# Kernel tuning notes

Measured on AMD Instinct MI355X. Metric: run time of the kernel, lower is better.

The kernel has to match this reference:

```python
import jax, jax.numpy as jnp
import numpy as np

DIM = 256


def _layernorm(x, g, b, eps=1e-5):
    mu = x.mean(-1, keepdims=True)
    var = x.var(-1, keepdims=True)  # biased, matches torch LayerNorm
    return (x - mu) / jnp.sqrt(var + eps) * g + b


def _softmax_kernel(d, proj, ratio, eps=1e-4):
    # FAVOR+ softmax kernel feature map: ratio*(exp(d@proj^T - |d|^2/2) + eps)
    dd = jnp.einsum('bnc,fc->bnf', d, proj)
    diag = 0.5 * jnp.sum(d * d, axis=-1, keepdims=True)
    return ratio * (jnp.exp(dd - diag) + eps)


def setup_inputs() -> dict:
    d = DIM
    rng = np.random.default_rng(0)
    # gaussian orthogonal random matrix (nb_features == dim -> single QR block)
    qmat, _ = np.linalg.qr(rng.standard_normal((d, d)))
    mult = np.linalg.norm(rng.standard_normal((d, d)), axis=1)
    proj = (np.diag(mult) @ qmat.T).astype(np.float32)

    key = jax.random.key(0)
    ks = jax.random.split(key, 8)

    def lin(k, o, i):
        s = 1.0 / np.sqrt(i)
        return jax.random.uniform(k, (o, i), jnp.float32, -s, s)

    return {
        'x': jax.random.normal(ks[0], (8, d, 64, 64), jnp.float32),
        'proj': jnp.asarray(proj),
        'wq': lin(ks[1], d, d), 'bq': jnp.zeros((d,), jnp.float32),
        'wk': lin(ks[2], d, d), 'bk': jnp.zeros((d,), jnp.float32),
        'wa': lin(ks[3], d, d), 'ba': jnp.zeros((d,), jnp.float32),
        'g1': jnp.ones((d,), jnp.float32), 'b1': jnp.zeros((d,), jnp.float32),
        'g2': jnp.ones((d,), jnp.float32), 'b2': jnp.zeros((d,), jnp.float32),
        'w1': lin(ks[4], 4 * d, d), 'fb1': jnp.zeros((4 * d,), jnp.float32),
        'w2': lin(ks[5], d, 4 * d), 'fb2': jnp.zeros((d,), jnp.float32),
    }


def reference(x, proj, wq, bq, wk, bk, wa, ba, g1, b1, g2, b2, w1, fb1, w2, fb2):
    B, C, H, W = x.shape
    N = H * W
    t = x.reshape(B, C, N).transpose(0, 2, 1)  # [B, N, C] tokens
    shortcut = t
    h = _layernorm(t, g1, b1)
    # 1x1 convs == per-token linears (conv weight [out,in,1,1] -> [out,in])
    q = h @ wq.T + bq
    k = h @ wk.T + bk
    v = h @ wa.T + ba
    # F.normalize(p=2, dim=channel, eps=5e-5): x / max(||x||, eps)
    qn = q / jnp.maximum(jnp.linalg.norm(q, axis=-1, keepdims=True), 5e-5)
    kn = k / jnp.maximum(jnp.linalg.norm(k, axis=-1, keepdims=True), 5e-5)
    ratio = proj.shape[0] ** -0.5
    qp = _softmax_kernel(qn, proj, ratio)  # [B, N, F]
    kp = _softmax_kernel(kn, proj, ratio)  # [B, N, F]
    # linear attention (single head, squeezed)
    k_sum = kp.sum(axis=1)                                    # [B, F]
    D_inv = 1.0 / jnp.einsum('bnf,bf->bn', qp, k_sum)         # [B, N]
    ctx = jnp.einsum('bnf,bnc->bfc', kp, v)                   # [B, F, C]
    out = jnp.einsum('bfc,bnf,bn->bnc', ctx, qp, D_inv)       # [B, N, C]
    t = shortcut + out
    h2 = _layernorm(t, g2, b2)
    m = jax.nn.gelu(h2 @ w1.T + fb1, approximate=False) @ w2.T + fb2
    t = t + m
    return t.transpose(0, 2, 1).reshape(B, C, H, W)
```

## Files before the change

### kernel.cpp

```cpp
#include <hip/hip_runtime.h>
#include <hip/hip_bf16.h>
#include <math.h>

typedef __hip_bfloat16 bf16;
typedef __attribute__((ext_vector_type(8))) short short8;
typedef __attribute__((ext_vector_type(4))) short short4v;
typedef __attribute__((ext_vector_type(4))) unsigned short ushort4v;
typedef __attribute__((ext_vector_type(4))) float f32x4;
typedef unsigned int u32;

#define BB 8
#define CC 256
#define NTOKB 4096
#define FF 256
#define HIDDEN 1024
#define NTOK (BB*NTOKB)

#if defined(__has_builtin)
#if __has_builtin(__builtin_amdgcn_global_load_lds)
#define HAS_GLL 1
#endif
#endif
#ifndef HAS_GLL
#define HAS_GLL 0
#endif

__device__ __forceinline__ float bf2f(bf16 x) { return __bfloat162float(x); }
__device__ __forceinline__ bf16 f2bf(float x) { return __float2bfloat16(x); }
__device__ __forceinline__ float clampf(float v, float lo, float hi) {
    return fminf(fmaxf(v, lo), hi);
}
__device__ __forceinline__ float s2f(short s) {
    unsigned int u = ((unsigned int)(unsigned short)s) << 16;
    float f; __builtin_memcpy(&f, &u, 4); return f;
}
__device__ __forceinline__ unsigned short f2bits(float v) {
    bf16 h = f2bf(v);
    unsigned short b; __builtin_memcpy(&b, &h, 2); return b;
}

__device__ __forceinline__ float fast_erf(float x) {
    float ax = fabsf(x);
    float t = __builtin_amdgcn_rcpf(fmaf(0.3275911f, ax, 1.f));
    float p = fmaf(t, 1.061405429f, -1.453152027f);
    p = fmaf(t, p, 1.421413741f);
    p = fmaf(t, p, -0.284496736f);
    p = fmaf(t, p, 0.254829592f);
    p = p * t;
    float e = __expf(-ax * ax);
    float r = fmaf(-p, e, 1.f);
    return x < 0.f ? -r : r;
}

#if HAS_GLL
__device__ __forceinline__ void gll16(const void* g, void* l) {
    __builtin_amdgcn_global_load_lds(
        (const __attribute__((address_space(1))) u32*)g,
        (__attribute__((address_space(3))) u32*)l, 16, 0, 0);
}
#endif

__device__ __forceinline__ float ldin(const void* p, size_t i, int fp32mode) {
    float v = fp32mode ? ((const float*)p)[i] : __bfloat162float(((const bf16*)p)[i]);
    if (!(v == v)) v = 0.f;
    return clampf(v, -1e4f, 1e4f);
}

__device__ __forceinline__ float wave_sum(float v) {
#pragma unroll
    for (int off = 32; off > 0; off >>= 1) v += __shfl_xor(v, off, 64);
    return v;
}

__global__ void detect_mode(const void* __restrict__ x, int* __restrict__ flag) {
    int i = threadIdx.x;
    float vb = __bfloat162float(((const bf16*)x)[(size_t)i * 37 + 1]);
    int bad = (!(vb == vb)) || (fabsf(vb) > 1e4f);
    unsigned long long m = __ballot(bad);
    if (i == 0) *flag = (m != 0ull) ? 1 : 0;
}

__global__ void convw_all(const void* __restrict__ wq, const void* __restrict__ wk,
                          const void* __restrict__ wa, const void* __restrict__ proj,
                          const void* __restrict__ w1, const void* __restrict__ w2,
                          const void* __restrict__ bq, const void* __restrict__ bk,
                          const void* __restrict__ ba,
                          bf16* __restrict__ dst, float* __restrict__ bqkv,
                          const int* __restrict__ mode) {
    int fp32 = *mode;
    int i = blockIdx.x * 256 + threadIdx.x;
    if (i < 786432) {
        const void* src; size_t off;
        if (i < 262144) {
            int seg = i >> 16; off = (size_t)(i & 65535);
            src = seg == 0 ? wq : seg == 1 ? wk : seg == 2 ? wa : proj;
        } else if (i < 524288) { src = w1; off = (size_t)(i - 262144); }
        else { src = w2; off = (size_t)(i - 524288); }
        dst[i] = f2bf(ldin(src, off, fp32));
    } else if (i < 787200) {
        int j = i - 786432;
        const void* s = j < 256 ? bq : j < 512 ? bk : ba;
        bqkv[j] = ldin(s, (size_t)(j & 255), fp32);
    }
}


__global__ void transpose_in_off(const void* __restrict__ X, bf16* __restrict__ T,
                                 const int* __restrict__ mode, size_t eoff) {
    __shared__ float tile[32][33];
    int fp32 = *mode;
    int n0 = blockIdx.x * 32, c0 = blockIdx.y * 32;
    int tx = threadIdx.x, ty = threadIdx.y;
    for (int i = ty; i < 32; i += 8)
        tile[i][tx] = ldin(X, eoff + (size_t)(c0 + i) * NTOKB + n0 + tx, fp32);
    __syncthreads();
    for (int i = ty; i < 32; i += 8)
        T[(size_t)(n0 + i) * CC + c0 + tx] = f2bf(tile[tx][i]);
}

__global__ void transpose_out_off(const bf16* __restrict__ T, void* __restrict__ O,
                                  const int* __restrict__ mode, size_t eoff) {
    __shared__ float tile[32][33];
    int fp32 = *mode;
    int c0 = blockIdx.x * 32, n0 = blockIdx.y * 32;
    int tx = threadIdx.x, ty = threadIdx.y;
    for (int i = ty; i < 32; i += 8)
        tile[i][tx] = bf2f(T[(size_t)(n0 + i) * CC + c0 + tx]);
    __syncthreads();
    for (int i = ty; i < 32; i += 8) {
        size_t idx = eoff + (size_t)(c0 + i) * NTOKB + n0 + tx;
        float v = tile[tx][i];
        if (fp32) ((float*)O)[idx] = v; else ((bf16*)O)[idx] = f2bf(v);
    }
}

__global__ void transpose_in_z(const void* __restrict__ X, bf16* __restrict__ T,
                               const int* __restrict__ mode) {
    __shared__ float tile[32][33];
    int fp32 = *mode;
    int b = blockIdx.z;
    int n0 = blockIdx.x * 32, c0 = blockIdx.y * 32;
    int tx = threadIdx.x, ty = threadIdx.y;
    size_t eoff = (size_t)b * CC * NTOKB;
    for (int i = ty; i < 32; i += 8)
        tile[i][tx] = ldin(X, eoff + (size_t)(c0 + i) * NTOKB + n0 + tx, fp32);
    __syncthreads();
    for (int i = ty; i < 32; i += 8)
        T[((size_t)b * NTOKB + n0 + i) * CC + c0 + tx] = f2bf(tile[tx][i]);
}

__global__ void layernorm_k(const bf16* __restrict__ X, const void* __restrict__ g,
                            const void* __restrict__ bta, bf16* __restrict__ Y,
                            const int* __restrict__ mode) {
    int fp32 = *mode;
    int t = blockIdx.x * 4 + (threadIdx.x >> 6);
    int lane = threadIdx.x & 63;
    const bf16* row = X + (size_t)t * CC;
    float v[4], s = 0.f, s2 = 0.f;
#pragma unroll
    for (int j = 0; j < 4; j++) {
        v[j] = bf2f(row[lane + 64 * j]);
        s += v[j]; s2 += v[j] * v[j];
    }
    s = wave_sum(s); s2 = wave_sum(s2);
    float mu = s * (1.f / CC);
    float var = s2 * (1.f / CC) - mu * mu;
    float rstd = rsqrtf(fmaxf(var, 0.f) + 1e-5f);
    bf16* yrow = Y + (size_t)t * CC;
#pragma unroll
    for (int j = 0; j < 4; j++) {
        int c = lane + 64 * j;
        yrow[c] = f2bf((v[j] - mu) * rstd * ldin(g, c, fp32) + ldin(bta, c, fp32));
    }
}

__global__ void layernorm_v(const bf16* __restrict__ X, const void* __restrict__ g,
                            const void* __restrict__ bta, bf16* __restrict__ Y,
                            const int* __restrict__ mode) {
    int fp32 = *mode;
    int t = blockIdx.x * 4 + (threadIdx.x >> 6);
    int lane = threadIdx.x & 63;
    const short* row = (const short*)X + (size_t)t * CC;
    short4v u = *(const short4v*)&row[lane * 4];
    float v[4], s = 0.f, s2 = 0.f;
#pragma unroll
    for (int j = 0; j < 4; j++) { v[j] = s2f(u[j]); s += v[j]; s2 += v[j] * v[j]; }
    s = wave_sum(s); s2 = wave_sum(s2);
    float mu = s * (1.f / CC);
    float var = s2 * (1.f / CC) - mu * mu;
    float rstd = rsqrtf(fmaxf(var, 0.f) + 1e-5f);
    ushort4v o;
#pragma unroll
    for (int j = 0; j < 4; j++) {
        int c = lane * 4 + j;
        o[j] = f2bits((v[j] - mu) * rstd * ldin(g, c, fp32) + ldin(bta, c, fp32));
    }
    *(ushort4v*)((unsigned short*)Y + (size_t)t * CC + lane * 4) = o;
}

__global__ void rownorm_k(bf16* __restrict__ Q, float* __restrict__ DIAG) {
    int t = blockIdx.x * 4 + (threadIdx.x >> 6);
    int lane = threadIdx.x & 63;
    bf16* row = Q + (size_t)t * CC;
    float v[4], s2 = 0.f;
#pragma unroll
    for (int j = 0; j < 4; j++) { v[j] = bf2f(row[lane + 64 * j]); s2 += v[j] * v[j]; }
    s2 = wave_sum(s2);
    float nrm = sqrtf(fmaxf(s2, 0.f));
    float scale = 1.f / fmaxf(nrm, 5e-5f);
#pragma unroll
    for (int j = 0; j < 4; j++) row[lane + 64 * j] = f2bf(v[j] * scale);
    if (lane == 0) DIAG[t] = 0.5f * s2 * scale * scale;
}

__global__ void rownorm_v(bf16* __restrict__ Q, float* __restrict__ DIAG) {
    int t = blockIdx.x * 4 + (threadIdx.x >> 6);
    int lane = threadIdx.x & 63;
    short* row = (short*)Q + (size_t)t * CC;
    short4v u = *(const short4v*)&row[lane * 4];
    float v[4], s2 = 0.f;
#pragma unroll
    for (int j = 0; j < 4; j++) { v[j] = s2f(u[j]); s2 += v[j] * v[j]; }
    s2 = wave_sum(s2);
    float nrm = sqrtf(fmaxf(s2, 0.f));
    float scale = 1.f / fmaxf(nrm, 5e-5f);
    ushort4v o;
#pragma unroll
    for (int j = 0; j < 4; j++) o[j] = f2bits(v[j] * scale);
    *(ushort4v*)&row[lane * 4] = o;
    if (lane == 0) DIAG[t] = 0.5f * s2 * scale * scale;
}


template <int EPI>
__global__ void gemm_nt(const bf16* __restrict__ A, const void* __restrict__ Bw,
                        const void* __restrict__ bias, const float* __restrict__ diag,
                        const bf16* __restrict__ resid, bf16* __restrict__ Cm,
                        int M, int Nn, int Kk, const int* __restrict__ mode) {
    __shared__ float As[32][33];
    __shared__ float Bs[32][33];
    int fp32 = *mode;
    int tx = threadIdx.x, ty = threadIdx.y;
    int n0 = blockIdx.x * 32, m0 = blockIdx.y * 32;
    int tid = ty * 16 + tx;
    int lr = tid >> 5, lc = tid & 31;
    float acc[2][2] = {{0.f, 0.f}, {0.f, 0.f}};
    for (int k0 = 0; k0 < Kk; k0 += 32) {
#pragma unroll
        for (int i = 0; i < 4; i++) {
            int r = lr + 8 * i;
            As[r][lc] = bf2f(A[(size_t)(m0 + r) * Kk + k0 + lc]);
            Bs[r][lc] = ldin(Bw, (size_t)(n0 + r) * Kk + k0 + lc, fp32);
        }
        __syncthreads();
#pragma unroll
        for (int kk = 0; kk < 32; kk++) {
            float a0 = As[ty][kk], a1 = As[ty + 16][kk];
            float b0 = Bs[tx][kk], b1 = Bs[tx + 16][kk];
            acc[0][0] += a0 * b0; acc[0][1] += a0 * b1;
            acc[1][0] += a1 * b0; acc[1][1] += a1 * b1;
        }
        __syncthreads();
    }
#pragma unroll
    for (int i = 0; i < 2; i++)
#pragma unroll
        for (int j = 0; j < 2; j++) {
            int m = m0 + ty + 16 * i, n = n0 + tx + 16 * j;
            float v = acc[i][j];
            if (EPI == 0) {
                v = clampf(v + ldin(bias, n, fp32), -1e6f, 1e6f);
            } else if (EPI == 1) {
                v = fminf(0.0625f * (expf(fminf(v - diag[m], 60.f)) + 1e-4f), 1e8f);
            } else if (EPI == 2) {
                v += ldin(bias, n, fp32);
                v = 0.5f * v * (1.f + erff(v * 0.70710678118654752f));
            } else if (EPI == 3) {
                v += ldin(bias, n, fp32);
                v = clampf(v + bf2f(resid[(size_t)m * Nn + n]), -1e6f, 1e6f);
            }
            Cm[(size_t)m * Nn + n] = f2bf(v);
        }
}

__global__ void gemm_ctx_fb(const bf16* __restrict__ KP, const bf16* __restrict__ V,
                            float* __restrict__ CTX) {
    __shared__ float Ks[32][33];
    __shared__ float Vs[32][33];
    int c0 = blockIdx.x * 32, f0 = blockIdx.y * 32;
    int tx = threadIdx.x, ty = threadIdx.y;
    int tid = ty * 16 + tx, lr = tid >> 5, lc = tid & 31;
    float acc[2][2] = {{0.f, 0.f}, {0.f, 0.f}};
    for (int n0 = 0; n0 < NTOKB; n0 += 32) {
#pragma unroll
        for (int i = 0; i < 4; i++) {
            int r = lr + 8 * i;
            Ks[r][lc] = bf2f(KP[(size_t)(n0 + r) * FF + f0 + lc]);
            Vs[r][lc] = bf2f(V[(size_t)(n0 + r) * CC + c0 + lc]);
        }
        __syncthreads();
#pragma unroll
        for (int kk = 0; kk < 32; kk++) {
            float a0 = Ks[kk][ty], a1 = Ks[kk][ty + 16];
            float b0 = Vs[kk][tx], b1 = Vs[kk][tx + 16];
            acc[0][0] += a0 * b0; acc[0][1] += a0 * b1;
            acc[1][0] += a1 * b0; acc[1][1] += a1 * b1;
        }
        __syncthreads();
    }
#pragma unroll
    for (int i = 0; i < 2; i++)
#pragma unroll
        for (int j = 0; j < 2; j++)
            CTX[(size_t)(f0 + ty + 16 * i) * CC + c0 + tx + 16 * j] =
                clampf(acc[i][j], -1e18f, 1e18f);
}

__global__ void gemm_attnout_fb(const bf16* __restrict__ QP, const float* __restrict__ CTX,
                                const float* __restrict__ DINV, bf16* __restrict__ T) {
    __shared__ float As[32][33];
    __shared__ float Bs[32][33];
    int c0 = blockIdx.x * 32, m0 = blockIdx.y * 32;
    int tx = threadIdx.x, ty = threadIdx.y;
    int tid = ty * 16 + tx, lr = tid >> 5, lc = tid & 31;
    float acc[2][2] = {{0.f, 0.f}, {0.f, 0.f}};
    for (int k0 = 0; k0 < FF; k0 += 32) {
#pragma unroll
        for (int i = 0; i < 4; i++) {
            int r = lr + 8 * i;
            As[r][lc] = bf2f(QP[(size_t)(m0 + r) * FF + k0 + lc]);
            Bs[r][lc] = CTX[(size_t)(k0 + r) * CC + c0 + lc];
        }
        __syncthreads();
#pragma unroll
        for (int kk = 0; kk < 32; kk++) {
            float a0 = As[ty][kk], a1 = As[ty + 16][kk];
            float b0 = Bs[kk][tx], b1 = Bs[kk][tx + 16];
            acc[0][0] += a0 * b0; acc[0][1] += a0 * b1;
            acc[1][0] += a1 * b0; acc[1][1] += a1 * b1;
        }
        __syncthreads();
    }
#pragma unroll
    for (int i = 0; i < 2; i++)
#pragma unroll
        for (int j = 0; j < 2; j++) {
            int t = m0 + ty + 16 * i;
            size_t idx = (size_t)t * CC + c0 + tx + 16 * j;
            float addv = clampf(acc[i][j] * DINV[t], -1e6f, 1e6f);
            T[idx] = f2bf(bf2f(T[idx]) + addv);
        }
}

__global__ void colsum_k(const bf16* __restrict__ KP, float* __restrict__ KPART) {
    int chunk = blockIdx.x;
    int f = threadIdx.x;
    const bf16* base = KP + (size_t)chunk * 128 * FF + f;
    float acc = 0.f;
    for (int i = 0; i < 128; i++) acc += bf2f(base[(size_t)i * FF]);
    KPART[(size_t)chunk * FF + f] = acc;
}

__global__ void ksum_reduce(const float* __restrict__ KPART, float* __restrict__ KSUM) {
    int f = threadIdx.x;
    float acc = 0.f;
#pragma unroll
    for (int c = 0; c < 32; c++) acc += KPART[(size_t)c * FF + f];
    KSUM[f] = acc;
}

__global__ void dinv_k(const bf16* __restrict__ QP, const float* __restrict__ KSUM,
                       float* __restrict__ DINV) {
    int t = blockIdx.x * 4 + (threadIdx.x >> 6);
    int lane = threadIdx.x & 63;
    const bf16* row = QP + (size_t)t * FF;
    float s = 0.f;
#pragma unroll
    for (int j = 0; j < 4; j++) { int c = lane + 64 * j; s += bf2f(row[c]) * KSUM[c]; }
    s = wave_sum(s);
    if (lane == 0) DINV[t] = fminf(1.f / fmaxf(s, 1e-30f), 1e6f);
}

template <int BM, int BN, int EPI, bool TRANSC>
__global__ __launch_bounds__(256) void mgemm(
    const bf16* __restrict__ A, int lda, long long aZ,
    const void* __restrict__ Bv, int ldb, long long bZ,
    const void* __restrict__ bias, const float* __restrict__ diag,
    const float* __restrict__ dinv,
    bf16* __restrict__ Cb, int ldc,
    bf16* __restrict__ Cb2, bf16* __restrict__ Cb3, float* __restrict__ Cf,
    int MperZ, int Kc, int nchunk, const int* __restrict__ mode)
{
    constexpr int MI = BM / 32;
    constexpr int NI = BN / 32;
    __shared__ short As[2][BM][32];
    __shared__ short Bs[2][BN][32];
    int fp32 = *mode;
    int z = blockIdx.z;
    int bl = z / nchunk;
    int chunk = z - bl * nchunk;
    const short* Ag = (const short*)A + (size_t)bl * aZ;
    const short* Bg = (const short*)Bv + (size_t)bl * bZ;

    int bx = blockIdx.x, by = blockIdx.y;
    if ((gridDim.y & 7) == 0) {
        int NB = gridDim.x;
        int flat = by * NB + bx;
        int grp = flat / (8 * NB);
        int rem = flat - grp * 8 * NB;
        by = grp * 8 + (rem & 7);
        bx = rem >> 3;
    }
    int n0 = bx * BN, m0 = by * BM;

    int tid = threadIdx.x;
    int lane = tid & 63, wave = tid >> 6;
    int wm = wave >> 1, wn = wave & 1;
    int row16 = lane & 15, quad = lane >> 4;
    int lrow = lane >> 2, lcol = (lane & 3) * 8;

    f32x4 acc[MI][NI];
#pragma unroll
    for (int i = 0; i < MI; i++)
#pragma unroll
        for (int j = 0; j < NI; j++) acc[i][j] = {0.f, 0.f, 0.f, 0.f};

    const int arb = wave * (BM / 4);
    const int brb = wave * (BN / 4);

    int kBase = chunk * Kc;
    int nt = Kc >> 5;

    auto stage = [&](int b, int kb) {
#pragma unroll
        for (int t = 0; t < BM / 64; t++) {
            int rbase = arb + t * 16;
            const short* gsrc = &Ag[(size_t)(m0 + rbase + lrow) * lda + kb + lcol];
#if HAS_GLL
            gll16(gsrc, &As[b][rbase][0]);
#else
            *(short8*)&As[b][rbase + lrow][lcol] = *(const short8*)gsrc;
#endif
        }
#pragma unroll
        for (int t = 0; t < BN / 64; t++) {
            int rbase = brb + t * 16;
            const short* gsrc = &Bg[(size_t)(n0 + rbase + lrow) * ldb + kb + lcol];
#if HAS_GLL
            gll16(gsrc, &Bs[b][rbase][0]);
#else
            *(short8*)&Bs[b][rbase + lrow][lcol] = *(const short8*)gsrc;
#endif
        }
    };

    auto compute = [&](int b) {
        short8 af[MI], bfr[NI];
#pragma unroll
        for (int i = 0; i < MI; i++)
            af[i] = *(const short8*)&As[b][wm * (BM / 2) + i * 16 + row16][quad * 8];
#pragma unroll
        for (int j = 0; j < NI; j++)
            bfr[j] = *(const short8*)&Bs[b][wn * (BN / 2) + j * 16 + row16][quad * 8];
#pragma unroll
        for (int i = 0; i < MI; i++)
#pragma unroll
            for (int j = 0; j < NI; j++)
                acc[i][j] = __builtin_amdgcn_mfma_f32_16x16x32_bf16(af[i], bfr[j], acc[i][j], 0, 0, 0);
    };

    stage(0, kBase);
    __syncthreads();

    int cur = 0;
    for (int t = 0; t + 1 < nt; ++t) {
        stage(cur ^ 1, kBase + (t + 1) * 32);
        compute(cur);
        __syncthreads();
        cur ^= 1;
    }
    compute(cur);

    float bv[NI];
    if (EPI == 0 || EPI == 2 || EPI == 3 || EPI == 8) {
#pragma unroll
        for (int j = 0; j < NI; j++)
            bv[j] = ldin(bias, n0 + wn * (BN / 2) + j * 16 + row16, fp32);
    } else if (EPI == 6) {
#pragma unroll
        for (int j = 0; j < NI; j++)
            bv[j] = diag[n0 + wn * (BN / 2) + j * 16 + row16];
    } else {
#pragma unroll
        for (int j = 0; j < NI; j++) bv[j] = 0.f;
    }

#pragma unroll
    for (int i = 0; i < MI; i++) {
        int mb = m0 + wm * (BM / 2) + i * 16 + quad * 4;
        float dg[4] = {0.f, 0.f, 0.f, 0.f};
        if (EPI == 1) {
#pragma unroll
            for (int r = 0; r < 4; r++) dg[r] = diag[mb + r];
        }
        if (EPI == 7) {
#pragma unroll
            for (int r = 0; r < 4; r++) dg[r] = diag[(size_t)bl * MperZ + mb + r];
        }
        float dvv[4] = {0.f, 0.f, 0.f, 0.f};
        if (EPI == 5) {
#pragma unroll
            for (int r = 0; r < 4; r++) dvv[r] = dinv[(size_t)bl * MperZ + mb + r];
        }
#pragma unroll
        for (int j = 0; j < NI; j++) {
            int n = n0 + wn * (BN / 2) + j * 16 + row16;
            if (EPI == 6) {
                int seg = n0 >> 8;
                int c = n & 255;
                if (seg == 2) {
                    ushort4v pack;
#pragma unroll
                    for (int r = 0; r < 4; r++)
                        pack[r] = f2bits(clampf(acc[i][j][r] + bv[j], -1e6f, 1e6f));
                    int blq = mb >> 12, tb = mb & 4095;
                    *(ushort4v*)((unsigned short*)Cb3 +
                        (size_t)blq * CC * NTOKB + (size_t)c * NTOKB + tb) = pack;
                } else {
                    bf16* dst = seg ? Cb2 : Cb;
#pragma unroll
                    for (int r = 0; r < 4; r++) {
                        float v = clampf(acc[i][j][r] + bv[j], -1e6f, 1e6f);
                        dst[(size_t)(mb + r) * CC + c] = f2bf(v);
                    }
                }
            } else if (EPI == 7) {
                if (bl == 1) {
                    ushort4v pack;
#pragma unroll
                    for (int r = 0; r < 4; r++) {
                        float v = fminf(0.0625f * (__expf(fminf(acc[i][j][r] - dg[r], 60.f)) + 1e-4f), 1e8f);
                        pack[r] = f2bits(v);
                    }
                    int blq = mb >> 12, tb = mb & 4095;
                    *(ushort4v*)((unsigned short*)Cb2 +
                        (size_t)blq * CC * NTOKB + (size_t)n * NTOKB + tb) = pack;
                } else {
#pragma unroll
                    for (int r = 0; r < 4; r++) {
                        float v = fminf(0.0625f * (__expf(fminf(acc[i][j][r] - dg[r], 60.f)) + 1e-4f), 1e8f);
                        Cb[(size_t)(mb + r) * ldc + n] = f2bf(v);
                    }
                }
            } else if (EPI == 8) {
                int blq = mb >> 12, tb = mb & 4095;
                if (fp32) {
                    f32x4 o;
#pragma unroll
                    for (int r = 0; r < 4; r++) {
                        float v = acc[i][j][r] + bv[j];
                        v = clampf(v + bf2f(Cb[(size_t)(mb + r) * ldc + n]), -1e6f, 1e6f);
                        o[r] = bf2f(f2bf(v));
                    }
                    *(f32x4*)((float*)Cb3 + ((size_t)blq * CC + n) * NTOKB + tb) = o;
                } else {
                    ushort4v pack;
#pragma unroll
                    for (int r = 0; r < 4; r++) {
                        float v = acc[i][j][r] + bv[j];
                        v = clampf(v + bf2f(Cb[(size_t)(mb + r) * ldc + n]), -1e6f, 1e6f);
                        pack[r] = f2bits(v);
                    }
                    *(ushort4v*)((unsigned short*)Cb3 + ((size_t)blq * CC + n) * NTOKB + tb) = pack;
                }
            } else if (TRANSC) {
                ushort4v pack;
#pragma unroll
                for (int r = 0; r < 4; r++) {
                    float v = acc[i][j][r];
                    if (EPI == 0) {
                        v = clampf(v + bv[j], -1e6f, 1e6f);
                    } else {
                        v = fminf(0.0625f * (__expf(fminf(v - dg[r], 60.f)) + 1e-4f), 1e8f);
                    }
                    pack[r] = f2bits(v);
                }
                int blq = mb >> 12, tb = mb & 4095;
                *(ushort4v*)((unsigned short*)Cb +
                    (size_t)blq * CC * NTOKB + (size_t)n * NTOKB + tb) = pack;
            } else {
#pragma unroll
                for (int r = 0; r < 4; r++) {
                    int m = mb + r;
                    float v = acc[i][j][r];
                    if (EPI == 0) {
                        v = clampf(v + bv[j], -1e6f, 1e6f);
                        Cb[(size_t)m * ldc + n] = f2bf(v);
                    } else if (EPI == 1) {
                        v = fminf(0.0625f * (__expf(fminf(v - dg[r], 60.f)) + 1e-4f), 1e8f);
                        Cb[(size_t)m * ldc + n] = f2bf(v);
                    } else if (EPI == 2) {
                        v += bv[j];
                        v = 0.5f * v * (1.f + fast_erf(v * 0.70710678118654752f));
                        Cb[(size_t)m * ldc + n] = f2bf(v);
                    } else if (EPI == 3) {
                        v += bv[j];
                        size_t idx = (size_t)m * ldc + n;
                        v = clampf(v + bf2f(Cb[idx]), -1e6f, 1e6f);
                        Cb[idx] = f2bf(v);
                    } else if (EPI == 4) {
                        Cf[(size_t)z * MperZ + (size_t)m * ldc + n] = v;
                    } else if (EPI == 5) {
                        size_t mg = (size_t)bl * MperZ + m;
                        float addv = clampf(v * dvv[r], -1e6f, 1e6f);
                        size_t idx = mg * ldc + n;
                        Cb[idx] = f2bf(bf2f(Cb[idx]) + addv);
                    }
                }
            }
        }
    }
}

__global__ void reduce_ctx(const float* __restrict__ PART, bf16* __restrict__ CTXT) {
    int f = blockIdx.x;
    int bl = blockIdx.y;
    int c = threadIdx.x;
    float s = 0.f;
#pragma unroll
    for (int ch = 0; ch < 16; ch++)
        s += PART[(((size_t)bl * 16 + ch) * FF + f) * CC + c];
    s = clampf(s, -1e18f, 1e18f);
    CTXT[((size_t)bl * CC + c) * FF + f] = f2bf(s);
}

__global__ void colsum_t(const bf16* __restrict__ KPT, float* __restrict__ KSUM) {
    int bl = blockIdx.y;
    int f = blockIdx.x * 4 + (threadIdx.x >> 6);
    int lane = threadIdx.x & 63;
    const short* row = (const short*)KPT + ((size_t)bl * FF + f) * NTOKB;
    float s = 0.f;
    for (int i = lane * 8; i < NTOKB; i += 512) {
        short8 v = *(const short8*)&row[i];
#pragma unroll
        for (int j = 0; j < 8; j++) s += s2f(v[j]);
    }
    s = wave_sum(s);
    if (lane == 0) KSUM[(size_t)bl * FF + f] = s;
}

__global__ void dinv_v(const bf16* __restrict__ QP, const float* __restrict__ KSUM,
                       float* __restrict__ DINV) {
    int bl = blockIdx.y;
    int t = blockIdx.x * 4 + (threadIdx.x >> 6);
    int lane = threadIdx.x & 63;
    const short* row = (const short*)QP + ((size_t)bl * NTOKB + t) * FF;
    const float* ks = KSUM + (size_t)bl * FF;
    short4v u = *(const short4v*)&row[lane * 4];
    float s = 0.f;
#pragma unroll
    for (int j = 0; j < 4; j++) s += s2f(u[j]) * ks[lane * 4 + j];
    s = wave_sum(s);
    if (lane == 0) DINV[(size_t)bl * NTOKB + t] = fminf(1.f / fmaxf(s, 1e-30f), 1e6f);
}

extern "C" void kernel_launch(void* const* d_in, const int* in_sizes, int n_in,
                              void* d_out, int out_size, void* d_ws, size_t ws_size,
                              hipStream_t stream) {
    const void* x    = d_in[0];
    const void* proj = d_in[1];
    const void* wq   = d_in[2];
    const void* bq   = d_in[3];
    const void* wk   = d_in[4];
    const void* bk   = d_in[5];
    const void* wa   = d_in[6];
    const void* ba   = d_in[7];
    const void* g1   = d_in[8];
    const void* b1   = d_in[9];
    const void* g2   = d_in[10];
    const void* b2   = d_in[11];
    const void* w1   = d_in[12];
    const void* fb1  = d_in[13];
    const void* w2   = d_in[14];
    const void* fb2  = d_in[15];

    char* base = (char*)d_ws;
    const size_t MB = 1048576ull;
    const bool fast = ws_size >= 168 * MB;

    if (fast) {
        bf16* T    = (bf16*)base;
        bf16* Hs   = (bf16*)(base + 16 * MB);
        bf16* Qs   = (bf16*)(base + 32 * MB);
        bf16* Ks   = (bf16*)(base + 48 * MB);
        bf16* VT   = (bf16*)(base + 64 * MB);
        bf16* KPT  = (bf16*)(base + 80 * MB);
        bf16* MID  = (bf16*)(base + 96 * MB);
        float* PART = (float*)(base + 96 * MB);
        char* sm = base + 160 * MB;
        int* MODE = (int*)sm;
        float* DIAGQ = (float*)(sm + 1024);
        float* DIAGK = DIAGQ + NTOK;
        float* DINV  = DIAGK + NTOK;
        float* KSUM  = DINV + NTOK;
        bf16* CTXT   = (bf16*)(sm + 2 * MB);
        bf16* WB     = (bf16*)(sm + 4 * MB);
        float* BQKV  = (float*)(sm + 6 * MB);

        dim3 tb32(32, 8);
        detect_mode<<<1, 64, 0, stream>>>(x, MODE);
        convw_all<<<3075, 256, 0, stream>>>(wq, wk, wa, proj, w1, w2,
                                            bq, bk, ba, WB, BQKV, MODE);
        transpose_in_z<<<dim3(NTOKB / 32, CC / 32, BB), tb32, 0, stream>>>(x, T, MODE);

        layernorm_v<<<NTOK / 4, 256, 0, stream>>>(T, g1, b1, Hs, MODE);
        mgemm<128, 128, 6, false><<<dim3(6, 256, 1), 256, 0, stream>>>(
            Hs, 256, 0, WB, 256, 0, nullptr, BQKV, nullptr,
            Qs, 256, Ks, VT, nullptr, 0, 256, 1, MODE);
        rownorm_v<<<NTOK / 4, 256, 0, stream>>>(Qs, DIAGQ);
        rownorm_v<<<NTOK / 4, 256, 0, stream>>>(Ks, DIAGK);
        mgemm<128, 128, 7, false><<<dim3(2, 256, 2), 256, 0, stream>>>(
            Qs, 256, 8388608LL , WB + 196608, 256, 0,
            nullptr, DIAGQ, nullptr,
            Hs, 256, KPT, nullptr, nullptr, NTOK, 256, 1, MODE);
        bf16* QP = Hs;
        colsum_t<<<dim3(FF / 4, BB), 256, 0, stream>>>(KPT, KSUM);
        dinv_v<<<dim3(NTOKB / 4, BB), 256, 0, stream>>>(QP, KSUM, DINV);
        mgemm<64, 128, 4, false><<<dim3(2, 4, BB * 16), 256, 0, stream>>>(
            KPT, NTOKB, (long long)FF * NTOKB, VT, NTOKB, (long long)CC * NTOKB,
            nullptr, nullptr, nullptr,
            nullptr, CC, nullptr, nullptr, PART, FF * CC, 256, 16, MODE);
        reduce_ctx<<<dim3(FF, BB), 256, 0, stream>>>(PART, CTXT);
        mgemm<128, 64, 5, false><<<dim3(4, 32, BB), 256, 0, stream>>>(
            QP, 256, (long long)NTOKB * FF, CTXT, FF, (long long)CC * FF,
            nullptr, nullptr, DINV,
            T, 256, nullptr, nullptr, nullptr, NTOKB, 256, 1, MODE);
        layernorm_v<<<NTOK / 4, 256, 0, stream>>>(T, g2, b2, Hs, MODE);
        mgemm<128, 128, 2, false><<<dim3(8, 256, 1), 256, 0, stream>>>(
            Hs, 256, 0, WB + 262144, 256, 0, fb1, nullptr, nullptr,
            MID, 1024, nullptr, nullptr, nullptr, 0, 256, 1, MODE);
        mgemm<128, 128, 8, false><<<dim3(2, 256, 1), 256, 0, stream>>>(
            MID, 1024, 0, WB + 524288, 1024, 0, fb2, nullptr, nullptr,
            T, 256, nullptr, (bf16*)d_out, nullptr, 0, 1024, 1, MODE);
        return;
    }

    bf16* Tb   = (bf16*)(base);
    bf16* Hb   = (bf16*)(base + 2 * MB);
    bf16* Qb   = (bf16*)(base + 4 * MB);
    bf16* Kb   = (bf16*)(base + 6 * MB);
    bf16* Vb   = (bf16*)(base + 8 * MB);
    bf16* QPb  = (bf16*)(base + 2 * MB);
    bf16* KPb  = (bf16*)(base + 4 * MB);
    bf16* MIDb = (bf16*)(base + 2 * MB);
    bf16* H2b  = (bf16*)(base + 10 * MB);
    char* sm   = base + 12 * MB;
    int*   MODE  = (int*)sm;
    float* DIAGQ = (float*)(sm + 256);
    float* DIAGK = DIAGQ + NTOKB;
    float* DINV  = DIAGK + NTOKB;
    float* KSUM  = DINV + NTOKB;
    float* KPART = KSUM + FF;
    float* CTX   = KPART + 32 * FF;

    dim3 tb32(32, 8);
    dim3 tb16(16, 16);
    dim3 gq(CC / 32, NTOKB / 32);

    detect_mode<<<1, 64, 0, stream>>>(x, MODE);

    for (int b = 0; b < BB; b++) {
        size_t eoff = (size_t)b * CC * NTOKB;
        transpose_in_off<<<dim3(NTOKB / 32, CC / 32), tb32, 0, stream>>>(x, Tb, MODE, eoff);
        layernorm_k<<<NTOKB / 4, 256, 0, stream>>>(Tb, g1, b1, Hb, MODE);
        gemm_nt<0><<<gq, tb16, 0, stream>>>(Hb, wq, bq, nullptr, nullptr, Qb, NTOKB, CC, CC, MODE);
        gemm_nt<0><<<gq, tb16, 0, stream>>>(Hb, wk, bk, nullptr, nullptr, Kb, NTOKB, CC, CC, MODE);
        gemm_nt<0><<<gq, tb16, 0, stream>>>(Hb, wa, ba, nullptr, nullptr, Vb, NTOKB, CC, CC, MODE);
        rownorm_k<<<NTOKB / 4, 256, 0, stream>>>(Qb, DIAGQ);
        rownorm_k<<<NTOKB / 4, 256, 0, stream>>>(Kb, DIAGK);
        gemm_nt<1><<<gq, tb16, 0, stream>>>(Qb, proj, nullptr, DIAGQ, nullptr, QPb, NTOKB, FF, CC, MODE);
        gemm_nt<1><<<gq, tb16, 0, stream>>>(Kb, proj, nullptr, DIAGK, nullptr, KPb, NTOKB, FF, CC, MODE);
        colsum_k<<<32, 256, 0, stream>>>(KPb, KPART);
        ksum_reduce<<<1, 256, 0, stream>>>(KPART, KSUM);
        dinv_k<<<NTOKB / 4, 256, 0, stream>>>(QPb, KSUM, DINV);
        gemm_ctx_fb<<<dim3(CC / 32, FF / 32), tb16, 0, stream>>>(KPb, Vb, CTX);
        gemm_attnout_fb<<<gq, tb16, 0, stream>>>(QPb, CTX, DINV, Tb);
        layernorm_k<<<NTOKB / 4, 256, 0, stream>>>(Tb, g2, b2, H2b, MODE);
        gemm_nt<2><<<dim3(HIDDEN / 32, NTOKB / 32), tb16, 0, stream>>>(H2b, w1, fb1, nullptr, nullptr, MIDb, NTOKB, HIDDEN, CC, MODE);
        gemm_nt<3><<<gq, tb16, 0, stream>>>(MIDb, w2, fb2, nullptr, Tb, Tb, NTOKB, CC, HIDDEN, MODE);
        transpose_out_off<<<dim3(CC / 32, NTOKB / 32), tb32, 0, stream>>>(Tb, d_out, MODE, eoff);
    }
}
```

Before: 383.6 us.

## Fuse input transpose with layernorm and fold row normalization into feature GEMM

Replaces the separate input transpose and first layernorm with one kernel that loads a 256x32 tile, computes per-token statistics in shared memory, and writes both the token copy and the normalized activations. The q/k row normalization no longer rewrites Q and K. It stores only a per-row scale, which the projection GEMM epilogue applies before the exponential. GEMM staging also uses precomputed incrementing pointers in place of recomputed addresses. This removes a full pass over the activations and two read-modify-write passes, at the cost of a large shared tile per block (about 34KB) that may limit occupancy, and a rounding difference because normalization now happens after the bf16 matmul.

```diff
diff --git a/kernel.cpp b/kernel.cpp
--- a/kernel.cpp
+++ b/kernel.cpp
@@ -104,6 +104,59 @@
     }
 }
 
+__global__ __launch_bounds__(256) void trans_ln(const void* __restrict__ X,
+        const void* __restrict__ g, const void* __restrict__ bta,
+        bf16* __restrict__ T, bf16* __restrict__ H,
+        const int* __restrict__ mode) {
+    __shared__ float tile[CC][33];
+    __shared__ float ps[8][32], ps2[8][32];
+    __shared__ float mu_s[32], rs_s[32];
+    int fp32 = *mode;
+    int b = blockIdx.y;
+    int n0 = blockIdx.x * 32;
+    int tx = threadIdx.x & 31, ty = threadIdx.x >> 5;
+    size_t eoff = (size_t)b * CC * NTOKB;
+    for (int c0 = 0; c0 < CC; c0 += 32)
+        for (int i = ty; i < 32; i += 8)
+            tile[c0 + i][tx] = ldin(X, eoff + (size_t)(c0 + i) * NTOKB + n0 + tx, fp32);
+    __syncthreads();
+    {
+        float s = 0.f, s2 = 0.f;
+#pragma unroll 8
+        for (int c = ty * 32; c < ty * 32 + 32; c++) {
+            float v = tile[c][tx]; s += v; s2 += v * v;
+        }
+        ps[ty][tx] = s; ps2[ty][tx] = s2;
+    }
+    __syncthreads();
+    if (threadIdx.x < 32) {
+        float s = 0.f, s2 = 0.f;
+#pragma unroll
+        for (int p = 0; p < 8; p++) { s += ps[p][threadIdx.x]; s2 += ps2[p][threadIdx.x]; }
+        float mu = s * (1.f / CC);
+        float var = s2 * (1.f / CC) - mu * mu;
+        mu_s[threadIdx.x] = mu;
+        rs_s[threadIdx.x] = rsqrtf(fmaxf(var, 0.f) + 1e-5f);
+    }
+    __syncthreads();
+    int token = threadIdx.x >> 3;
+    int cbase = (threadIdx.x & 7) * 32;
+    float mu = mu_s[token], rstd = rs_s[token];
+    size_t rowoff = ((size_t)b * NTOKB + n0 + token) * CC + cbase;
+    for (int cc = 0; cc < 32; cc += 4) {
+        ushort4v tpack, hpack;
+#pragma unroll
+        for (int q = 0; q < 4; q++) {
+            int c = cbase + cc + q;
+            float v = tile[c][token];
+            tpack[q] = f2bits(v);
+            hpack[q] = f2bits((v - mu) * rstd * ldin(g, c, fp32) + ldin(bta, c, fp32));
+        }
+        *(ushort4v*)((unsigned short*)T + rowoff + cc) = tpack;
+        *(ushort4v*)((unsigned short*)H + rowoff + cc) = hpack;
+    }
+}
+
 
 __global__ void transpose_in_off(const void* __restrict__ X, bf16* __restrict__ T,
                                  const int* __restrict__ mode, size_t eoff) {
@@ -134,21 +187,6 @@
     }
 }
 
-__global__ void transpose_in_z(const void* __restrict__ X, bf16* __restrict__ T,
-                               const int* __restrict__ mode) {
-    __shared__ float tile[32][33];
-    int fp32 = *mode;
-    int b = blockIdx.z;
-    int n0 = blockIdx.x * 32, c0 = blockIdx.y * 32;
-    int tx = threadIdx.x, ty = threadIdx.y;
-    size_t eoff = (size_t)b * CC * NTOKB;
-    for (int i = ty; i < 32; i += 8)
-        tile[i][tx] = ldin(X, eoff + (size_t)(c0 + i) * NTOKB + n0 + tx, fp32);
-    __syncthreads();
-    for (int i = ty; i < 32; i += 8)
-        T[((size_t)b * NTOKB + n0 + i) * CC + c0 + tx] = f2bf(tile[tx][i]);
-}
-
 __global__ void layernorm_k(const bf16* __restrict__ X, const void* __restrict__ g,
                             const void* __restrict__ bta, bf16* __restrict__ Y,
                             const int* __restrict__ mode) {
@@ -213,22 +251,22 @@
     if (lane == 0) DIAG[t] = 0.5f * s2 * scale * scale;
 }
 
-__global__ void rownorm_v(bf16* __restrict__ Q, float* __restrict__ DIAG) {
+__global__ void rowscale_v(const bf16* __restrict__ Q, float* __restrict__ SCALE,
+                           float* __restrict__ DIAG) {
     int t = blockIdx.x * 4 + (threadIdx.x >> 6);
     int lane = threadIdx.x & 63;
-    short* row = (short*)Q + (size_t)t * CC;
+    const short* row = (const short*)Q + (size_t)t * CC;
     short4v u = *(const short4v*)&row[lane * 4];
-    float v[4], s2 = 0.f;
-#pragma unroll
-    for (int j = 0; j < 4; j++) { v[j] = s2f(u[j]); s2 += v[j] * v[j]; }
+    float s2 = 0.f;
+#pragma unroll
+    for (int j = 0; j < 4; j++) { float v = s2f(u[j]); s2 += v * v; }
     s2 = wave_sum(s2);
-    float nrm = sqrtf(fmaxf(s2, 0.f));
-    float scale = 1.f / fmaxf(nrm, 5e-5f);
-    ushort4v o;
-#pragma unroll
-    for (int j = 0; j < 4; j++) o[j] = f2bits(v[j] * scale);
-    *(ushort4v*)&row[lane * 4] = o;
-    if (lane == 0) DIAG[t] = 0.5f * s2 * scale * scale;
+    if (lane == 0) {
+        float nrm = sqrtf(fmaxf(s2, 0.f));
+        float scale = 1.f / fmaxf(nrm, 5e-5f);
+        SCALE[t] = scale;
+        DIAG[t] = 0.5f * s2 * scale * scale;
+    }
 }
 
 
@@ -431,26 +469,33 @@
     int kBase = chunk * Kc;
     int nt = Kc >> 5;
 
-    auto stage = [&](int b, int kb) {
+    const short* aptr[BM / 64];
+    const short* bptr[BN / 64];
+#pragma unroll
+    for (int t = 0; t < BM / 64; t++)
+        aptr[t] = &Ag[(size_t)(m0 + arb + t * 16 + lrow) * lda + kBase + lcol];
+#pragma unroll
+    for (int t = 0; t < BN / 64; t++)
+        bptr[t] = &Bg[(size_t)(n0 + brb + t * 16 + lrow) * ldb + kBase + lcol];
+
+    auto stage = [&](int b) {
 #pragma unroll
         for (int t = 0; t < BM / 64; t++) {
-            int rbase = arb + t * 16;
-            const short* gsrc = &Ag[(size_t)(m0 + rbase + lrow) * lda + kb + lcol];
 #if HAS_GLL
-            gll16(gsrc, &As[b][rbase][0]);
+            gll16(aptr[t], &As[b][arb + t * 16][0]);
 #else
-            *(short8*)&As[b][rbase + lrow][lcol] = *(const short8*)gsrc;
+            *(short8*)&As[b][arb + t * 16 + lrow][lcol] = *(const short8*)aptr[t];
 #endif
+            aptr[t] += 32;
         }
 #pragma unroll
         for (int t = 0; t < BN / 64; t++) {
-            int rbase = brb + t * 16;
-            const short* gsrc = &Bg[(size_t)(n0 + rbase + lrow) * ldb + kb + lcol];
 #if HAS_GLL
-            gll16(gsrc, &Bs[b][rbase][0]);
+            gll16(bptr[t], &Bs[b][brb + t * 16][0]);
 #else
-            *(short8*)&Bs[b][rbase + lrow][lcol] = *(const short8*)gsrc;
+            *(short8*)&Bs[b][brb + t * 16 + lrow][lcol] = *(const short8*)bptr[t];
 #endif
+            bptr[t] += 32;
         }
     };
 
@@ -469,12 +514,12 @@
                 acc[i][j] = __builtin_amdgcn_mfma_f32_16x16x32_bf16(af[i], bfr[j], acc[i][j], 0, 0, 0);
     };
 
-    stage(0, kBase);
+    stage(0);
     __syncthreads();
 
     int cur = 0;
     for (int t = 0; t + 1 < nt; ++t) {
-        stage(cur ^ 1, kBase + (t + 1) * 32);
+        stage(cur ^ 1);
         compute(cur);
         __syncthreads();
         cur ^= 1;
@@ -508,7 +553,7 @@
             for (int r = 0; r < 4; r++) dg[r] = diag[(size_t)bl * MperZ + mb + r];
         }
         float dvv[4] = {0.f, 0.f, 0.f, 0.f};
-        if (EPI == 5) {
+        if (EPI == 5 || EPI == 7) {
 #pragma unroll
             for (int r = 0; r < 4; r++) dvv[r] = dinv[(size_t)bl * MperZ + mb + r];
         }
@@ -539,7 +584,7 @@
                     ushort4v pack;
 #pragma unroll
                     for (int r = 0; r < 4; r++) {
-                        float v = fminf(0.0625f * (__expf(fminf(acc[i][j][r] - dg[r], 60.f)) + 1e-4f), 1e8f);
+                        float v = fminf(0.0625f * (__expf(fminf(acc[i][j][r] * dvv[r] - dg[r], 60.f)) + 1e-4f), 1e8f);
                         pack[r] = f2bits(v);
                     }
                     int blq = mb >> 12, tb = mb & 4095;
@@ -548,7 +593,7 @@
                 } else {
 #pragma unroll
                     for (int r = 0; r < 4; r++) {
-                        float v = fminf(0.0625f * (__expf(fminf(acc[i][j][r] - dg[r], 60.f)) + 1e-4f), 1e8f);
+                        float v = fminf(0.0625f * (__expf(fminf(acc[i][j][r] * dvv[r] - dg[r], 60.f)) + 1e-4f), 1e8f);
                         Cb[(size_t)(mb + r) * ldc + n] = f2bf(v);
                     }
                 }
@@ -703,25 +748,25 @@
         float* DIAGK = DIAGQ + NTOK;
         float* DINV  = DIAGK + NTOK;
         float* KSUM  = DINV + NTOK;
+        float* SCALEQ = KSUM + BB * FF;
+        float* SCALEK = SCALEQ + NTOK;
         bf16* CTXT   = (bf16*)(sm + 2 * MB);
         bf16* WB     = (bf16*)(sm + 4 * MB);
         float* BQKV  = (float*)(sm + 6 * MB);
 
-        dim3 tb32(32, 8);
         detect_mode<<<1, 64, 0, stream>>>(x, MODE);
         convw_all<<<3075, 256, 0, stream>>>(wq, wk, wa, proj, w1, w2,
                                             bq, bk, ba, WB, BQKV, MODE);
-        transpose_in_z<<<dim3(NTOKB / 32, CC / 32, BB), tb32, 0, stream>>>(x, T, MODE);
-
-        layernorm_v<<<NTOK / 4, 256, 0, stream>>>(T, g1, b1, Hs, MODE);
+        trans_ln<<<dim3(NTOKB / 32, BB), 256, 0, stream>>>(x, g1, b1, T, Hs, MODE);
+
         mgemm<128, 128, 6, false><<<dim3(6, 256, 1), 256, 0, stream>>>(
             Hs, 256, 0, WB, 256, 0, nullptr, BQKV, nullptr,
             Qs, 256, Ks, VT, nullptr, 0, 256, 1, MODE);
-        rownorm_v<<<NTOK / 4, 256, 0, stream>>>(Qs, DIAGQ);
-        rownorm_v<<<NTOK / 4, 256, 0, stream>>>(Ks, DIAGK);
+        rowscale_v<<<NTOK / 4, 256, 0, stream>>>(Qs, SCALEQ, DIAGQ);
+        rowscale_v<<<NTOK / 4, 256, 0, stream>>>(Ks, SCALEK, DIAGK);
         mgemm<128, 128, 7, false><<<dim3(2, 256, 2), 256, 0, stream>>>(
             Qs, 256, 8388608LL , WB + 196608, 256, 0,
-            nullptr, DIAGQ, nullptr,
+            nullptr, DIAGQ, SCALEQ,
             Hs, 256, KPT, nullptr, nullptr, NTOK, 256, 1, MODE);
         bf16* QP = Hs;
         colsum_t<<<dim3(FF / 4, BB), 256, 0, stream>>>(KPT, KSUM);
```

After: 389.4 us. About the same (+1.5%).
